# Optimization experiments

Hardware: AMD Instinct MI355X
Metric: run time of the kernel (lower is better)

The kernel has to match this reference:

```python
import jax, jax.numpy as jnp
import numpy as np

B, T, F, H = 2048, 256, 64, 128


def setup_inputs() -> dict:
    key = jax.random.key(0)
    ks = jax.random.split(key, 9)
    s = 0.1  # small init scale for stable recurrence
    return {
        "x": jax.random.normal(ks[0], (B, T, F), dtype=jnp.float32),
        "W_ih": jax.random.normal(ks[1], (4 * H, F), dtype=jnp.float32) * s,
        "W_hh": jax.random.normal(ks[2], (4 * H, H), dtype=jnp.float32) * s,
        "b_ih": jax.random.normal(ks[3], (4 * H,), dtype=jnp.float32) * s,
        "b_hh": jax.random.normal(ks[4], (4 * H,), dtype=jnp.float32) * s,
        "W1": jax.random.normal(ks[5], (32, H), dtype=jnp.float32) * s,
        "b1": jax.random.normal(ks[6], (32,), dtype=jnp.float32) * s,
        "W2": jax.random.normal(ks[7], (1, 32), dtype=jnp.float32) * s,
        "b2": jax.random.normal(ks[8], (1,), dtype=jnp.float32) * s,
    }


def reference(x, W_ih, W_hh, b_ih, b_hh, W1, b1, W2, b2):
    # Single-layer LSTM (PyTorch gate order i, f, g, o), take last hidden state.
    Bsz, Tlen, _ = x.shape
    Hdim = W_hh.shape[1]
    xt = jnp.swapaxes(x, 0, 1)  # [T, B, F]
    bias = b_ih + b_hh  # [4H]

    def step(carry, xb):
        h, c = carry
        gates = xb @ W_ih.T + h @ W_hh.T + bias  # [B, 4H]
        i, f, g, o = jnp.split(gates, 4, axis=-1)
        i = jax.nn.sigmoid(i)
        f = jax.nn.sigmoid(f)
        g = jnp.tanh(g)
        o = jax.nn.sigmoid(o)
        c = f * c + i * g
        h = o * jnp.tanh(c)
        return (h, c), None

    h0 = jnp.zeros((Bsz, Hdim), dtype=x.dtype)
    c0 = jnp.zeros((Bsz, Hdim), dtype=x.dtype)
    (h_last, _), _ = jax.lax.scan(step, (h0, c0), xt)

    # head: Linear(H,32) -> ReLU -> Linear(32,1) -> Sigmoid -> squeeze(-1)
    z = jax.nn.relu(h_last @ W1.T + b1)
    return jax.nn.sigmoid(z @ W2.T + b2)[:, 0]
```

## Files before the change

kernel.cpp:

```cpp
#include <hip/hip_runtime.h>


#define Bsz   2048
#define Tlen  256
#define Fdim  64
#define Hdim  128
#define ROWS  8
#define NTH   512
#define TILE_E 512
#define NKT   6
#define BUF_E (NKT * TILE_E)

using bf16x8 = __attribute__((ext_vector_type(8))) __bf16;
using f32x4  = __attribute__((ext_vector_type(4))) float;

__device__ __forceinline__ float fast_rcp(float x) {
#if __has_builtin(__builtin_amdgcn_rcpf)
    return __builtin_amdgcn_rcpf(x);
#else
    return 1.0f / x;
#endif
}
__device__ __forceinline__ float fast_exp2(float x) {
#if __has_builtin(__builtin_amdgcn_exp2f)
    return __builtin_amdgcn_exp2f(x);
#else
    return exp2f(x);
#endif
}
__device__ __forceinline__ float fsig(float x) {
    return fast_rcp(1.0f + fast_exp2(-1.4426950408889634f * x));
}
__device__ __forceinline__ float ftanh(float x) {
    float e = fast_exp2(-2.8853900817779268f * x);
    return (1.0f - e) * fast_rcp(1.0f + e);
}

__device__ __forceinline__ bf16x8 cvt8(float4 a, float4 b) {
    bf16x8 r;
    r[0]=(__bf16)a.x; r[1]=(__bf16)a.y; r[2]=(__bf16)a.z; r[3]=(__bf16)a.w;
    r[4]=(__bf16)b.x; r[5]=(__bf16)b.y; r[6]=(__bf16)b.z; r[7]=(__bf16)b.w;
    return r;
}

__device__ __forceinline__ int frag_elem(int row, int k) {
    return (k >> 5) * TILE_E + ((((k >> 3) & 3) * 16 + row) * 8) + (k & 7);
}

__global__ __launch_bounds__(NTH, 2)
void lstm_fused(const float* __restrict__ x,
                const float* __restrict__ W_ih,
                const float* __restrict__ W_hh,
                const float* __restrict__ b_ih,
                const float* __restrict__ b_hh,
                const float* __restrict__ W1,
                const float* __restrict__ b1,
                const float* __restrict__ W2,
                const float* __restrict__ b2,
                float* __restrict__ out)
{
    __shared__ __bf16 Abuf[2][BUF_E];
    __shared__ float  hlast[ROWS * Hdim];
    __shared__ float  zbuf[ROWS * 32];

    const int tid  = threadIdx.x;
    const int w    = tid >> 6;
    const int lane = tid & 63;
    const int quad = lane >> 4;
    const int l16  = lane & 15;
    const int b0   = blockIdx.x * ROWS;
    const bool hiq = (quad >= 2);

    bf16x8 bwx[2][4], bwh[4][4];
    #pragma unroll
    for (int kt = 0; kt < NKT; ++kt) {
        const int k0 = kt * 32 + quad * 8;
        #pragma unroll
        for (int g = 0; g < 4; ++g) {
            const int n = g * Hdim + w * 16 + l16;
            const float* p = (kt < 2) ? (W_ih + (size_t)n * Fdim + k0)
                                      : (W_hh + (size_t)n * Hdim + (k0 - Fdim));
            float4 lo = *(const float4*)p;
            float4 hi = *(const float4*)(p + 4);
            bf16x8 r = cvt8(lo, hi);
            if (kt < 2) bwx[kt][g] = r; else bwh[kt - 2][g] = r;
        }
    }
    float biasv[4];
    #pragma unroll
    for (int g = 0; g < 4; ++g) {
        const int n = g * Hdim + w * 16 + l16;
        biasv[g] = b_ih[n] + b_hh[n];
    }

    const bool sx_on  = tid < 256;
    const int  sx_row = tid & 7;
    const int  sx_fp  = (tid >> 3) & 31;
    const int  f0     = 2 * sx_fp;
    const float* xrp  = x + (size_t)(b0 + sx_row) * (Tlen * Fdim) + f0;
    const int sx_e0 = frag_elem(sx_row,     f0);
    const int sx_e1 = frag_elem(sx_row + 8, f0);

    const int r0  = (quad >> 1) * 2;
    const int brb = (quad & 1) * 4 + r0;
    const int hc  = 16 * w + l16;
    const int h_e0a = frag_elem(brb,         Fdim + hc);
    const int h_e0b = frag_elem(brb + 8,     Fdim + hc);
    const int h_e1a = frag_elem(brb + 1,     Fdim + hc);
    const int h_e1b = frag_elem(brb + 1 + 8, Fdim + hc);

    #pragma unroll
    for (int i = 0; i < BUF_E / NTH; ++i)
        Abuf[0][tid + i * NTH] = (__bf16)0.0f;
    __syncthreads();
    float2 xpA = make_float2(0.f, 0.f);
    float2 xpB = make_float2(0.f, 0.f);
    if (sx_on) {
        float2 v1 = *(const float2*)(xrp + Fdim);
        __bf16 a1[2] = {(__bf16)v1.x, (__bf16)v1.y};
        *(uint*)&Abuf[0][sx_e0] = *(uint*)a1;
        *(uint*)&Abuf[0][sx_e1] = *(uint*)a1;
        xpA = *(const float2*)(xrp + 2 * Fdim);
        xpB = *(const float2*)(xrp + 3 * Fdim);
    }
    f32x4 xacc[4];
    {
        const float* x0p = x + (size_t)(b0 + (l16 & 7)) * (Tlen * Fdim) + quad * 8;
        float4 a0 = *(const float4*)(x0p);
        float4 a1 = *(const float4*)(x0p + 4);
        float4 a2 = *(const float4*)(x0p + 32);
        float4 a3 = *(const float4*)(x0p + 36);
        bf16x8 xi0 = cvt8(a0, a1), xi1 = cvt8(a2, a3);
        #pragma unroll
        for (int g = 0; g < 4; ++g) {
            xacc[g] = (f32x4){biasv[g], biasv[g], biasv[g], biasv[g]};
            xacc[g] = __builtin_amdgcn_mfma_f32_16x16x32_bf16(xi0, bwx[0][g], xacc[g], 0, 0, 0);
            xacc[g] = __builtin_amdgcn_mfma_f32_16x16x32_bf16(xi1, bwx[1][g], xacc[g], 0, 0, 0);
        }
    }
    __syncthreads();

    float cc0 = 0.0f, cc1 = 0.0f;

    auto step = [&](int t, const __bf16* __restrict__ rb,
                    __bf16* __restrict__ wbf, float2& xstage) {
        bf16x8 hf[4];
        #pragma unroll
        for (int kt = 0; kt < 4; ++kt)
            hf[kt] = *(const bf16x8*)&rb[(2 + kt) * TILE_E + lane * 8];
        bf16x8 xf0 = *(const bf16x8*)&rb[lane * 8];
        bf16x8 xf1 = *(const bf16x8*)&rb[TILE_E + lane * 8];

        float2 xcur = xstage;
        if (sx_on && (t + 4) < Tlen)
            xstage = *(const float2*)(xrp + (size_t)(t + 4) * Fdim);

        f32x4 acc[4];
        #pragma unroll
        for (int g = 0; g < 4; ++g)
            acc[g] = __builtin_amdgcn_mfma_f32_16x16x32_bf16(hf[0], bwh[0][g], xacc[g], 0, 0, 0);
        #pragma unroll
        for (int kt = 1; kt < 4; ++kt) {
            #pragma unroll
            for (int g = 0; g < 4; ++g)
                acc[g] = __builtin_amdgcn_mfma_f32_16x16x32_bf16(hf[kt], bwh[kt][g], acc[g], 0, 0, 0);
        }

        {
            float iv = fsig (hiq ? acc[0][2] : acc[0][0]);
            float fv = fsig (hiq ? acc[1][2] : acc[1][0]);
            float gv = ftanh(hiq ? acc[2][2] : acc[2][0]);
            float ov = fsig (hiq ? acc[3][2] : acc[3][0]);
            cc0 = fv * cc0 + iv * gv;
            float h = ov * ftanh(cc0);
            __bf16 hb = (__bf16)h;
            wbf[h_e0a] = hb;
            wbf[h_e0b] = hb;
            if (t == Tlen - 1) hlast[brb * Hdim + hc] = h;
        }
        {
            float iv = fsig (hiq ? acc[0][3] : acc[0][1]);
            float fv = fsig (hiq ? acc[1][3] : acc[1][1]);
            float gv = ftanh(hiq ? acc[2][3] : acc[2][1]);
            float ov = fsig (hiq ? acc[3][3] : acc[3][1]);
            cc1 = fv * cc1 + iv * gv;
            float h = ov * ftanh(cc1);
            __bf16 hb = (__bf16)h;
            wbf[h_e1a] = hb;
            wbf[h_e1b] = hb;
            if (t == Tlen - 1) hlast[(brb + 1) * Hdim + hc] = h;
        }

        if ((t + 1) < Tlen) {
            #pragma unroll
            for (int g = 0; g < 4; ++g) {
                xacc[g] = (f32x4){biasv[g], biasv[g], biasv[g], biasv[g]};
                xacc[g] = __builtin_amdgcn_mfma_f32_16x16x32_bf16(xf0, bwx[0][g], xacc[g], 0, 0, 0);
                xacc[g] = __builtin_amdgcn_mfma_f32_16x16x32_bf16(xf1, bwx[1][g], xacc[g], 0, 0, 0);
            }
        }

        if (sx_on && (t + 2) < Tlen) {
            __bf16 xa[2] = {(__bf16)xcur.x, (__bf16)xcur.y};
            *(uint*)&wbf[sx_e0] = *(uint*)xa;
            *(uint*)&wbf[sx_e1] = *(uint*)xa;
        }

        asm volatile("s_waitcnt lgkmcnt(0)" ::: "memory");
        __builtin_amdgcn_s_barrier();
        __builtin_amdgcn_sched_barrier(0);
    };

    for (int t = 0; t < Tlen; t += 2) {
        step(t,     Abuf[0], Abuf[1], xpA);
        step(t + 1, Abuf[1], Abuf[0], xpB);
    }

    if (tid < ROWS * 32) {
        const int b = tid >> 5, n = tid & 31;
        const float4* w4 = (const float4*)(W1 + n * Hdim);
        const float4* h4 = (const float4*)(hlast + b * Hdim);
        float s = b1[n];
        #pragma unroll
        for (int kk = 0; kk < Hdim / 4; ++kk) {
            float4 wv = w4[kk];
            float4 hv = h4[kk];
            s += wv.x * hv.x + wv.y * hv.y + wv.z * hv.z + wv.w * hv.w;
        }
        zbuf[b * 32 + n] = fmaxf(s, 0.0f);
    }
    __syncthreads();
    if (tid < ROWS) {
        float s = b2[0];
        #pragma unroll
        for (int n = 0; n < 32; ++n) s += zbuf[tid * 32 + n] * W2[n];
        out[b0 + tid] = fsig(s);
    }
}

extern "C" void kernel_launch(void* const* d_in, const int* in_sizes, int n_in,
                              void* d_out, int out_size, void* d_ws, size_t ws_size,
                              hipStream_t stream) {
    const float* x    = (const float*)d_in[0];
    const float* W_ih = (const float*)d_in[1];
    const float* W_hh = (const float*)d_in[2];
    const float* b_ih = (const float*)d_in[3];
    const float* b_hh = (const float*)d_in[4];
    const float* W1   = (const float*)d_in[5];
    const float* b1   = (const float*)d_in[6];
    const float* W2   = (const float*)d_in[7];
    const float* b2   = (const float*)d_in[8];
    float* out = (float*)d_out;

    dim3 grid(Bsz / ROWS), block(NTH);
    lstm_fused<<<grid, block, 0, stream>>>(x, W_ih, W_hh, b_ih, b_hh, W1, b1, W2, b2, out);
}
```

Measured before the change: 343.6 us.

## Merge LSTM gate reciprocals algebraically and hoist next-step x MFMAs before activations

Rewrites the cell update so the sigmoid and tanh reciprocals combine into a single reciprocal for c and one for h. This cuts the rcp count per element from six to two on the serial critical path. The x-projection MFMAs for the next step and the x staging writes now issue before the activation math, with a sched_barrier, so the MFMA work overlaps the transcendental ALU work. It also feeds the bias directly as the MFMA accumulator instead of copying it into xacc. The combined-denominator form risks overflow or inf/inf NaN when the exponentials are large, for example with strongly negative gate pre-activations.

```diff
diff --git a/kernel.cpp b/kernel.cpp
--- a/kernel.cpp
+++ b/kernel.cpp
@@ -28,13 +28,8 @@
     return exp2f(x);
 #endif
 }
-__device__ __forceinline__ float fsig(float x) {
-    return fast_rcp(1.0f + fast_exp2(-1.4426950408889634f * x));
-}
-__device__ __forceinline__ float ftanh(float x) {
-    float e = fast_exp2(-2.8853900817779268f * x);
-    return (1.0f - e) * fast_rcp(1.0f + e);
-}
+#define LOG2E  1.4426950408889634f
+#define LOG2E2 2.8853900817779268f
 
 __device__ __forceinline__ bf16x8 cvt8(float4 a, float4 b) {
     bf16x8 r;
@@ -86,11 +81,12 @@
             if (kt < 2) bwx[kt][g] = r; else bwh[kt - 2][g] = r;
         }
     }
-    float biasv[4];
+    f32x4 biasf[4];
     #pragma unroll
     for (int g = 0; g < 4; ++g) {
         const int n = g * Hdim + w * 16 + l16;
-        biasv[g] = b_ih[n] + b_hh[n];
+        const float bv = b_ih[n] + b_hh[n];
+        biasf[g] = (f32x4){bv, bv, bv, bv};
     }
 
     const bool sx_on  = tid < 256;
@@ -133,9 +129,8 @@
         bf16x8 xi0 = cvt8(a0, a1), xi1 = cvt8(a2, a3);
         #pragma unroll
         for (int g = 0; g < 4; ++g) {
-            xacc[g] = (f32x4){biasv[g], biasv[g], biasv[g], biasv[g]};
-            xacc[g] = __builtin_amdgcn_mfma_f32_16x16x32_bf16(xi0, bwx[0][g], xacc[g], 0, 0, 0);
-            xacc[g] = __builtin_amdgcn_mfma_f32_16x16x32_bf16(xi1, bwx[1][g], xacc[g], 0, 0, 0);
+            f32x4 tmp = __builtin_amdgcn_mfma_f32_16x16x32_bf16(xi0, bwx[0][g], biasf[g], 0, 0, 0);
+            xacc[g]   = __builtin_amdgcn_mfma_f32_16x16x32_bf16(xi1, bwx[1][g], tmp, 0, 0, 0);
         }
     }
     __syncthreads();
@@ -166,44 +161,61 @@
                 acc[g] = __builtin_amdgcn_mfma_f32_16x16x32_bf16(hf[kt], bwh[kt][g], acc[g], 0, 0, 0);
         }
 
+        if ((t + 1) < Tlen) {
+            #pragma unroll
+            for (int g = 0; g < 4; ++g) {
+                f32x4 tmp = __builtin_amdgcn_mfma_f32_16x16x32_bf16(xf0, bwx[0][g], biasf[g], 0, 0, 0);
+                xacc[g]   = __builtin_amdgcn_mfma_f32_16x16x32_bf16(xf1, bwx[1][g], tmp, 0, 0, 0);
+            }
+        }
+
+        if (sx_on && (t + 2) < Tlen) {
+            __bf16 xa[2] = {(__bf16)xcur.x, (__bf16)xcur.y};
+            *(uint*)&wbf[sx_e0] = *(uint*)xa;
+            *(uint*)&wbf[sx_e1] = *(uint*)xa;
+        }
+
+        __builtin_amdgcn_sched_barrier(0);
+
         {
-            float iv = fsig (hiq ? acc[0][2] : acc[0][0]);
-            float fv = fsig (hiq ? acc[1][2] : acc[1][0]);
-            float gv = ftanh(hiq ? acc[2][2] : acc[2][0]);
-            float ov = fsig (hiq ? acc[3][2] : acc[3][0]);
-            cc0 = fv * cc0 + iv * gv;
-            float h = ov * ftanh(cc0);
+            float gi = hiq ? acc[0][2] : acc[0][0];
+            float gf = hiq ? acc[1][2] : acc[1][0];
+            float gg = hiq ? acc[2][2] : acc[2][0];
+            float go = hiq ? acc[3][2] : acc[3][0];
+            float ei = fast_exp2(-LOG2E  * gi);
+            float ef = fast_exp2(-LOG2E  * gf);
+            float eg = fast_exp2(-LOG2E2 * gg);
+            float eo = fast_exp2(-LOG2E  * go);
+            float a = 1.0f + ef, b = 1.0f + ei, d = 1.0f + eg;
+            float bd  = b * d;
+            float num = cc0 * bd + a * (1.0f - eg);
+            cc0 = num * fast_rcp(a * bd);
+            float ec = fast_exp2(-LOG2E2 * cc0);
+            float h  = (1.0f - ec) * fast_rcp((1.0f + eo) * (1.0f + ec));
             __bf16 hb = (__bf16)h;
             wbf[h_e0a] = hb;
             wbf[h_e0b] = hb;
             if (t == Tlen - 1) hlast[brb * Hdim + hc] = h;
         }
         {
-            float iv = fsig (hiq ? acc[0][3] : acc[0][1]);
-            float fv = fsig (hiq ? acc[1][3] : acc[1][1]);
-            float gv = ftanh(hiq ? acc[2][3] : acc[2][1]);
-            float ov = fsig (hiq ? acc[3][3] : acc[3][1]);
-            cc1 = fv * cc1 + iv * gv;
-            float h = ov * ftanh(cc1);
+            float gi = hiq ? acc[0][3] : acc[0][1];
+            float gf = hiq ? acc[1][3] : acc[1][1];
+            float gg = hiq ? acc[2][3] : acc[2][1];
+            float go = hiq ? acc[3][3] : acc[3][1];
+            float ei = fast_exp2(-LOG2E  * gi);
+            float ef = fast_exp2(-LOG2E  * gf);
+            float eg = fast_exp2(-LOG2E2 * gg);
+            float eo = fast_exp2(-LOG2E  * go);
+            float a = 1.0f + ef, b = 1.0f + ei, d = 1.0f + eg;
+            float bd  = b * d;
+            float num = cc1 * bd + a * (1.0f - eg);
+            cc1 = num * fast_rcp(a * bd);
+            float ec = fast_exp2(-LOG2E2 * cc1);
+            float h  = (1.0f - ec) * fast_rcp((1.0f + eo) * (1.0f + ec));
             __bf16 hb = (__bf16)h;
             wbf[h_e1a] = hb;
             wbf[h_e1b] = hb;
             if (t == Tlen - 1) hlast[(brb + 1) * Hdim + hc] = h;
-        }
-
-        if ((t + 1) < Tlen) {
-            #pragma unroll
-            for (int g = 0; g < 4; ++g) {
-                xacc[g] = (f32x4){biasv[g], biasv[g], biasv[g], biasv[g]};
-                xacc[g] = __builtin_amdgcn_mfma_f32_16x16x32_bf16(xf0, bwx[0][g], xacc[g], 0, 0, 0);
-                xacc[g] = __builtin_amdgcn_mfma_f32_16x16x32_bf16(xf1, bwx[1][g], xacc[g], 0, 0, 0);
-            }
-        }
-
-        if (sx_on && (t + 2) < Tlen) {
-            __bf16 xa[2] = {(__bf16)xcur.x, (__bf16)xcur.y};
-            *(uint*)&wbf[sx_e0] = *(uint*)xa;
-            *(uint*)&wbf[sx_e1] = *(uint*)xa;
         }
 
         asm volatile("s_waitcnt lgkmcnt(0)" ::: "memory");
@@ -234,7 +246,8 @@
         float s = b2[0];
         #pragma unroll
         for (int n = 0; n < 32; ++n) s += zbuf[tid * 32 + n] * W2[n];
-        out[b0 + tid] = fsig(s);
+        float e = fast_exp2(-LOG2E * s);
+        out[b0 + tid] = fast_rcp(1.0f + e);
     }
 }
 
```

Measured after the change: 342.9 us. No clear change (-0.2%).
